# Performance work log

Measured on AMD Instinct MI355X. Metric: run time of the kernel, lower is better.

## Reference

```python
import jax, jax.numpy as jnp
import numpy as np


def _mlp(h, W1, b1, W2, b2):
    # Linear -> ReLU -> Linear
    h = jax.nn.relu(h @ W1 + b1)
    return h @ W2 + b2


def setup_inputs() -> dict:
    key = jax.random.key(0)
    ks = jax.random.split(key, 8)
    N, E, DN, DE, H, O = 50000, 800000, 128, 64, 256, 128
    DIN = DN + DE  # 192
    s1 = 1.0 / np.sqrt(DIN)
    s2 = 1.0 / np.sqrt(H)
    return {
        "x": jax.random.normal(ks[0], (N, DN), dtype=jnp.float32),
        "edge_index": jax.random.randint(ks[1], (2, E), 0, N, dtype=jnp.int32),
        "edge_attr": jax.random.normal(ks[2], (E, DE), dtype=jnp.float32),
        "W1_out": jax.random.normal(ks[3], (DIN, H), dtype=jnp.float32) * s1,
        "b1_out": jnp.zeros((H,), dtype=jnp.float32),
        "W2_out": jax.random.normal(ks[4], (H, O), dtype=jnp.float32) * s2,
        "b2_out": jnp.zeros((O,), dtype=jnp.float32),
        "W1_in": jax.random.normal(ks[5], (DIN, H), dtype=jnp.float32) * s1,
        "b1_in": jnp.zeros((H,), dtype=jnp.float32),
        "W2_in": jax.random.normal(ks[6], (H, O), dtype=jnp.float32) * s2,
        "b2_in": jnp.zeros((O,), dtype=jnp.float32),
    }


def reference(x, edge_index, edge_attr, W1_out, b1_out, W2_out, b2_out,
              W1_in, b1_in, W2_in, b2_in):
    N = x.shape[0]
    row, col = edge_index[0], edge_index[1]
    # Shared gather + concat: [E, d_node + d_edge]
    msg_in = jnp.concatenate([x[col], edge_attr], axis=1)

    # flow_out: edges with row < col. Compute MLP densely, zero masked edges,
    # then scatter-sum -> identical math to masked gather + scatter-sum.
    m_out = (row < col).astype(x.dtype)[:, None]
    flow_out = _mlp(msg_in, W1_out, b1_out, W2_out, b2_out) * m_out
    flow_out = jax.ops.segment_sum(flow_out, row, num_segments=N)

    # flow_in: edges with row > col
    m_in = (row > col).astype(x.dtype)[:, None]
    flow_in = _mlp(msg_in, W1_in, b1_in, W2_in, b2_in) * m_in
    flow_in = jax.ops.segment_sum(flow_in, row, num_segments=N)

    return jnp.concatenate((flow_in, flow_out), axis=1)  # [N, 2*O]
```

## Files before the change

kernel.cpp:

```cpp
#include <hip/hip_runtime.h>
#include <hip/hip_bf16.h>

typedef __attribute__((ext_vector_type(8))) short short8;
typedef __attribute__((ext_vector_type(4))) float f32x4;

#define DN   128
#define DE   64
#define DIN  192
#define HID  256
#define OUTD 128
#define TE   64
#define MSG_LD 200
#define H_LD   264
#define OUT_LD 132

static __device__ __forceinline__ unsigned short f2b(float f) {
    unsigned int u = __float_as_uint(f);
    u += 0x7fffu + ((u >> 16) & 1u);
    return (unsigned short)(u >> 16);
}

__global__ void pack_all_kernel(const float* __restrict__ W1o, const float* __restrict__ W1i,
                                const float* __restrict__ W2o, const float* __restrict__ W2i,
                                unsigned short* __restrict__ W1po, unsigned short* __restrict__ W1pi,
                                unsigned short* __restrict__ W2po, unsigned short* __restrict__ W2pi) {
    const int S1 = DIN * HID, S2 = HID * OUTD;
    int idx = blockIdx.x * blockDim.x + threadIdx.x;
    const float* W; unsigned short* Wp; int Ncols, j;
    if      (idx < S1)            { W = W1o; Wp = W1po; Ncols = HID;  j = idx; }
    else if (idx < 2*S1)          { W = W1i; Wp = W1pi; Ncols = HID;  j = idx - S1; }
    else if (idx < 2*S1 + S2)     { W = W2o; Wp = W2po; Ncols = OUTD; j = idx - 2*S1; }
    else if (idx < 2*S1 + 2*S2)   { W = W2i; Wp = W2pi; Ncols = OUTD; j = idx - 2*S1 - S2; }
    else return;
    int k = j / Ncols, n = j - k * Ncols;
    Wp[(((k >> 5) * Ncols + n) << 5) + (k & 31)] = f2b(W[j]);
}

__global__ __launch_bounds__(256)
void part_hist_kernel(const int* __restrict__ ei, int E, int N, int* __restrict__ hist) {
    int e = blockIdx.x * blockDim.x + threadIdx.x;
    if (e >= E) return;
    int r = ei[e], c = ei[E + e];
    if      (r < c) atomicAdd(&hist[r], 1);
    else if (r > c) atomicAdd(&hist[N + r], 1);
}

__global__ __launch_bounds__(1024)
void scan_kernel(const int* __restrict__ hist, int* __restrict__ cursor,
                 int* __restrict__ cnt, int N) {
    __shared__ int s_ws[16];
    __shared__ int s_run;
    const int tid = threadIdx.x, lane = tid & 63, wv = tid >> 6;
    const int b = blockIdx.x;
    const int* h = hist + (size_t)b * N;
    int* cu = cursor + (size_t)b * N;
    if (tid == 0) s_run = 0;
    __syncthreads();
    for (int base = 0; base < N; base += 1024) {
        int i = base + tid;
        int v = (i < N) ? h[i] : 0;
        int incl = v;
        #pragma unroll
        for (int d = 1; d < 64; d <<= 1) {
            int t = __shfl_up(incl, d, 64);
            if (lane >= d) incl += t;
        }
        if (lane == 63) s_ws[wv] = incl;
        __syncthreads();
        if (tid < 16) {
            int w = s_ws[tid];
            int wi = w;
            #pragma unroll
            for (int d = 1; d < 16; d <<= 1) {
                int t = __shfl_up(wi, d, 64);
                if (tid >= d) wi += t;
            }
            s_ws[tid] = wi - w;
        }
        __syncthreads();
        int excl = s_run + s_ws[wv] + incl - v;
        if (i < N) cu[i] = excl;
        __syncthreads();
        if (tid == 1023) s_run = excl + v;
        __syncthreads();
    }
    if (tid == 0) cnt[b] = s_run;
}

__global__ __launch_bounds__(256)
void reorder_kernel(const int* __restrict__ ei, int E, int N, int* __restrict__ cursor,
                    int* __restrict__ list_out, int* __restrict__ list_in) {
    int e = blockIdx.x * blockDim.x + threadIdx.x;
    if (e >= E) return;
    int r = ei[e], c = ei[E + e];
    if      (r < c) { int p = atomicAdd(&cursor[r], 1);            list_out[p] = e; }
    else if (r > c) { int p = atomicAdd(&cursor[(size_t)N + r], 1); list_in[p] = e; }
}

__global__ __launch_bounds__(256, 4)
void mlp_scatter_kernel(const float* __restrict__ x,
                        const int* __restrict__ ei,
                        const float* __restrict__ ea,
                        const unsigned short* __restrict__ W1p_out,
                        const unsigned short* __restrict__ W1p_in,
                        const float* __restrict__ b1_out,
                        const float* __restrict__ b1_in,
                        const unsigned short* __restrict__ W2p_out,
                        const unsigned short* __restrict__ W2p_in,
                        const float* __restrict__ b2_out,
                        const float* __restrict__ b2_in,
                        const int* __restrict__ list_out,
                        const int* __restrict__ list_in,
                        const int* __restrict__ cnt,
                        float* __restrict__ out,
                        int E, int nbpb) {
    __shared__ __align__(16) unsigned short s_buf[TE * H_LD];
    __shared__ int s_eid[TE], s_dest[TE], s_col[TE];

    const int branch = (blockIdx.x >= nbpb) ? 1 : 0;
    const int lb = blockIdx.x - branch * nbpb;
    const int count = cnt[branch];
    if (lb * TE >= count) return;
    const int* list            = branch ? list_in : list_out;
    const unsigned short* W1p  = branch ? W1p_in  : W1p_out;
    const float* b1            = branch ? b1_in   : b1_out;
    const unsigned short* W2p  = branch ? W2p_in  : W2p_out;
    const float* b2            = branch ? b2_in   : b2_out;
    const int colbase          = branch ? 0 : OUTD;

    const int tid = threadIdx.x;
    if (tid < TE) {
        int idx = lb * TE + tid;
        int e = (idx < count) ? list[idx] : -1;
        s_eid[tid]  = e;
        s_dest[tid] = (e >= 0) ? ei[e] : -1;
        s_col[tid]  = (e >= 0) ? ei[E + e] : 0;
    }
    __syncthreads();

    {
        const int le  = tid >> 2;
        const int sub = tid & 3;
        const int e   = s_eid[le];
        const long xbase = (long)s_col[le] * 32;
        const long ebase = (long)e * 16;
        #pragma unroll
        for (int j = 0; j < 12; ++j) {
            int q = sub + j * 4;
            float4 v = make_float4(0.f, 0.f, 0.f, 0.f);
            if (e >= 0) {
                if (j < 8) v = reinterpret_cast<const float4*>(x)[xbase + q];
                else       v = reinterpret_cast<const float4*>(ea)[ebase + (q - 32)];
            }
            unsigned int lo = (unsigned int)f2b(v.x) | ((unsigned int)f2b(v.y) << 16);
            unsigned int hi = (unsigned int)f2b(v.z) | ((unsigned int)f2b(v.w) << 16);
            *reinterpret_cast<uint2*>(&s_buf[le * MSG_LD + q * 4]) = make_uint2(lo, hi);
        }
    }
    __syncthreads();

    const int wave = tid >> 6;
    const int lane = tid & 63;
    const int ln   = lane & 15;
    const int quad = lane >> 4;

    f32x4 acc[4][4];
    {
        const int nbase = wave * 64;
        float bias[4];
        #pragma unroll
        for (int t = 0; t < 4; ++t) bias[t] = b1[nbase + t * 16 + ln];
        #pragma unroll
        for (int mt = 0; mt < 4; ++mt)
            #pragma unroll
            for (int t = 0; t < 4; ++t)
                acc[mt][t] = (f32x4){bias[t], bias[t], bias[t], bias[t]};
        #pragma unroll
        for (int kt = 0; kt < DIN / 32; ++kt) {
            short8 a[4], b[4];
            #pragma unroll
            for (int mt = 0; mt < 4; ++mt)
                a[mt] = *reinterpret_cast<const short8*>(
                    &s_buf[(mt * 16 + ln) * MSG_LD + kt * 32 + quad * 8]);
            #pragma unroll
            for (int t = 0; t < 4; ++t)
                b[t] = *reinterpret_cast<const short8*>(
                    &W1p[((kt * HID + nbase + t * 16 + ln) << 5) + quad * 8]);
            #pragma unroll
            for (int mt = 0; mt < 4; ++mt)
                #pragma unroll
                for (int t = 0; t < 4; ++t)
                    acc[mt][t] = __builtin_amdgcn_mfma_f32_16x16x32_bf16(a[mt], b[t], acc[mt][t], 0, 0, 0);
        }
    }
    __syncthreads();

    {
        const int nbase = wave * 64;
        #pragma unroll
        for (int mt = 0; mt < 4; ++mt)
            #pragma unroll
            for (int t = 0; t < 4; ++t) {
                int ncol = nbase + t * 16 + ln;
                #pragma unroll
                for (int r = 0; r < 4; ++r) {
                    int m = mt * 16 + quad * 4 + r;
                    float v = acc[mt][t][r];
                    s_buf[m * H_LD + ncol] = f2b(v > 0.f ? v : 0.f);
                }
            }
    }
    __syncthreads();

    f32x4 acc2[4][2];
    {
        const int nbase = wave * 32;
        float bias2[2];
        #pragma unroll
        for (int t = 0; t < 2; ++t) bias2[t] = b2[nbase + t * 16 + ln];
        #pragma unroll
        for (int mt = 0; mt < 4; ++mt)
            #pragma unroll
            for (int t = 0; t < 2; ++t)
                acc2[mt][t] = (f32x4){bias2[t], bias2[t], bias2[t], bias2[t]};
        #pragma unroll
        for (int kt = 0; kt < HID / 32; ++kt) {
            short8 a[4], b[2];
            #pragma unroll
            for (int mt = 0; mt < 4; ++mt)
                a[mt] = *reinterpret_cast<const short8*>(
                    &s_buf[(mt * 16 + ln) * H_LD + kt * 32 + quad * 8]);
            #pragma unroll
            for (int t = 0; t < 2; ++t)
                b[t] = *reinterpret_cast<const short8*>(
                    &W2p[((kt * OUTD + nbase + t * 16 + ln) << 5) + quad * 8]);
            #pragma unroll
            for (int mt = 0; mt < 4; ++mt)
                #pragma unroll
                for (int t = 0; t < 2; ++t)
                    acc2[mt][t] = __builtin_amdgcn_mfma_f32_16x16x32_bf16(a[mt], b[t], acc2[mt][t], 0, 0, 0);
        }
    }
    __syncthreads();

    float* s_outf = reinterpret_cast<float*>(s_buf);
    {
        const int nbase = wave * 32;
        #pragma unroll
        for (int mt = 0; mt < 4; ++mt)
            #pragma unroll
            for (int t = 0; t < 2; ++t)
                #pragma unroll
                for (int r = 0; r < 4; ++r)
                    s_outf[(mt * 16 + quad * 4 + r) * OUT_LD + nbase + t * 16 + ln] = acc2[mt][t][r];
    }
    __syncthreads();

    {
        const int c  = tid & 127;
        const int m0 = (tid >> 7) * 32;
        float run = 0.f;
        int cur = -1;
        #pragma unroll 8
        for (int m = m0; m < m0 + 32; ++m) {
            int d = s_dest[m];
            float v = s_outf[m * OUT_LD + c];
            if (d != cur) {
                if (cur >= 0) atomicAdd(&out[(size_t)cur * (2 * OUTD) + colbase + c], run);
                cur = d; run = 0.f;
            }
            if (d >= 0) run += v;
        }
        if (cur >= 0) atomicAdd(&out[(size_t)cur * (2 * OUTD) + colbase + c], run);
    }
}

extern "C" void kernel_launch(void* const* d_in, const int* in_sizes, int n_in,
                              void* d_out, int out_size, void* d_ws, size_t ws_size,
                              hipStream_t stream) {
    const float* x   = (const float*)d_in[0];
    const int*   ei  = (const int*)d_in[1];
    const float* ea  = (const float*)d_in[2];
    const float* W1o = (const float*)d_in[3];
    const float* b1o = (const float*)d_in[4];
    const float* W2o = (const float*)d_in[5];
    const float* b2o = (const float*)d_in[6];
    const float* W1i = (const float*)d_in[7];
    const float* b1i = (const float*)d_in[8];
    const float* W2i = (const float*)d_in[9];
    const float* b2i = (const float*)d_in[10];
    float* out = (float*)d_out;
    const int E = in_sizes[1] / 2;
    const int N = in_sizes[0] / DN;

    char* ws = (char*)d_ws;
    int* cnt      = (int*)ws;
    int* hist     = (int*)(ws + 64);
    int* cursor   = hist + 2 * (size_t)N;
    int* list_out = cursor + 2 * (size_t)N;
    int* list_in  = list_out + E;
    unsigned short* W1po = (unsigned short*)(list_in + E);
    unsigned short* W1pi = W1po + DIN * HID;
    unsigned short* W2po = W1pi + DIN * HID;
    unsigned short* W2pi = W2po + HID * OUTD;

    hipMemsetAsync(d_out, 0, (size_t)out_size * sizeof(float), stream);
    hipMemsetAsync(ws, 0, 64 + 2 * (size_t)N * sizeof(int), stream);

    const int packN = 2 * DIN * HID + 2 * HID * OUTD;
    pack_all_kernel<<<(packN + 255) / 256, 256, 0, stream>>>(
        W1o, W1i, W2o, W2i, W1po, W1pi, W2po, W2pi);

    part_hist_kernel<<<(E + 255) / 256, 256, 0, stream>>>(ei, E, N, hist);
    scan_kernel<<<2, 1024, 0, stream>>>(hist, cursor, cnt, N);
    reorder_kernel<<<(E + 255) / 256, 256, 0, stream>>>(ei, E, N, cursor, list_out, list_in);

    const int nbpb = (E + TE - 1) / TE;
    mlp_scatter_kernel<<<2 * nbpb, 256, 0, stream>>>(
        x, ei, ea, W1po, W1pi, b1o, b1i, W2po, W2pi, b2o, b2i,
        list_out, list_in, cnt, out, E, nbpb);
}
```

Measured before the change: 660.4 us.

## Pre-convert x to bf16, fuse prep kernels, parallelize scan, store interior segments

```diff
diff --git a/kernel.cpp b/kernel.cpp
--- a/kernel.cpp
+++ b/kernel.cpp
@@ -2,6 +2,7 @@
 #include <hip/hip_bf16.h>
 
 typedef __attribute__((ext_vector_type(8))) short short8;
+typedef __attribute__((ext_vector_type(8))) unsigned short ushort8;
 typedef __attribute__((ext_vector_type(4))) float f32x4;
 
 #define DN   128
@@ -20,85 +21,102 @@
     return (unsigned short)(u >> 16);
 }
 
-__global__ void pack_all_kernel(const float* __restrict__ W1o, const float* __restrict__ W1i,
-                                const float* __restrict__ W2o, const float* __restrict__ W2i,
-                                unsigned short* __restrict__ W1po, unsigned short* __restrict__ W1pi,
-                                unsigned short* __restrict__ W2po, unsigned short* __restrict__ W2pi) {
-    const int S1 = DIN * HID, S2 = HID * OUTD;
+__global__ __launch_bounds__(256)
+void prep_kernel(const float* __restrict__ W1o, const float* __restrict__ W1i,
+                 const float* __restrict__ W2o, const float* __restrict__ W2i,
+                 unsigned short* __restrict__ W1po, unsigned short* __restrict__ W1pi,
+                 unsigned short* __restrict__ W2po, unsigned short* __restrict__ W2pi,
+                 const int* __restrict__ ei, int E, int N, int* __restrict__ hist,
+                 const float* __restrict__ x, unsigned short* __restrict__ xb) {
+    const int S1 = DIN * HID, S2v = HID * OUTD;
+    const int PACKN = 2 * S1 + 2 * S2v;
     int idx = blockIdx.x * blockDim.x + threadIdx.x;
-    const float* W; unsigned short* Wp; int Ncols, j;
-    if      (idx < S1)            { W = W1o; Wp = W1po; Ncols = HID;  j = idx; }
-    else if (idx < 2*S1)          { W = W1i; Wp = W1pi; Ncols = HID;  j = idx - S1; }
-    else if (idx < 2*S1 + S2)     { W = W2o; Wp = W2po; Ncols = OUTD; j = idx - 2*S1; }
-    else if (idx < 2*S1 + 2*S2)   { W = W2i; Wp = W2pi; Ncols = OUTD; j = idx - 2*S1 - S2; }
-    else return;
-    int k = j / Ncols, n = j - k * Ncols;
-    Wp[(((k >> 5) * Ncols + n) << 5) + (k & 31)] = f2b(W[j]);
+    if (idx < PACKN) {
+        const float* W; unsigned short* Wp; int Nc, j;
+        if      (idx < S1)          { W = W1o; Wp = W1po; Nc = HID;  j = idx; }
+        else if (idx < 2*S1)        { W = W1i; Wp = W1pi; Nc = HID;  j = idx - S1; }
+        else if (idx < 2*S1 + S2v)  { W = W2o; Wp = W2po; Nc = OUTD; j = idx - 2*S1; }
+        else                        { W = W2i; Wp = W2pi; Nc = OUTD; j = idx - 2*S1 - S2v; }
+        int k = j / Nc, n = j - k * Nc;
+        Wp[(((k >> 5) * Nc + n) << 5) + (k & 31)] = f2b(W[j]);
+    } else if (idx < PACKN + E) {
+        int e = idx - PACKN;
+        int r = ei[e], c = ei[E + e];
+        if      (r < c) atomicAdd(&hist[r], 1);
+        else if (r > c) atomicAdd(&hist[N + r], 1);
+    } else {
+        int i = idx - PACKN - E;
+        if (i < N * DN / 8) {
+            float4 a = reinterpret_cast<const float4*>(x)[i * 2];
+            float4 b = reinterpret_cast<const float4*>(x)[i * 2 + 1];
+            ushort8 v = { f2b(a.x), f2b(a.y), f2b(a.z), f2b(a.w),
+                          f2b(b.x), f2b(b.y), f2b(b.z), f2b(b.w) };
+            reinterpret_cast<ushort8*>(xb)[i] = v;
+        }
+    }
+}
+
+__global__ __launch_bounds__(1024)
+void scan1_kernel(const int* __restrict__ hist, int* __restrict__ cursor,
+                  int* __restrict__ chunkSum, int N, int nch) {
+    __shared__ int s_ws[16];
+    const int br = blockIdx.x / nch, ch = blockIdx.x - br * nch;
+    const int tid = threadIdx.x, lane = tid & 63, wv = tid >> 6;
+    const int i = ch * 1024 + tid;
+    int v = (i < N) ? hist[(size_t)br * N + i] : 0;
+    int incl = v;
+    #pragma unroll
+    for (int d = 1; d < 64; d <<= 1) {
+        int t = __shfl_up(incl, d, 64);
+        if (lane >= d) incl += t;
+    }
+    if (lane == 63) s_ws[wv] = incl;
+    __syncthreads();
+    if (tid < 16) {
+        int w = s_ws[tid];
+        int wi = w;
+        #pragma unroll
+        for (int d = 1; d < 16; d <<= 1) {
+            int t = __shfl_up(wi, d, 64);
+            if (tid >= d) wi += t;
+        }
+        s_ws[tid] = wi - w;
+    }
+    __syncthreads();
+    int excl = s_ws[wv] + incl - v;
+    if (i < N) cursor[(size_t)br * N + i] = excl;
+    if (tid == 1023) chunkSum[br * nch + ch] = excl + v;
+}
+
+__global__ __launch_bounds__(128)
+void scan2_kernel(int* __restrict__ chunkSum, int* __restrict__ cnt, int nch) {
+    const int br = threadIdx.x >> 6, lane = threadIdx.x & 63;
+    int v = (lane < nch) ? chunkSum[br * nch + lane] : 0;
+    int incl = v;
+    #pragma unroll
+    for (int d = 1; d < 64; d <<= 1) {
+        int t = __shfl_up(incl, d, 64);
+        if (lane >= d) incl += t;
+    }
+    if (lane < nch) chunkSum[br * nch + lane] = incl - v;
+    if (lane == nch - 1) cnt[br] = incl;
 }
 
 __global__ __launch_bounds__(256)
-void part_hist_kernel(const int* __restrict__ ei, int E, int N, int* __restrict__ hist) {
-    int e = blockIdx.x * blockDim.x + threadIdx.x;
-    if (e >= E) return;
-    int r = ei[e], c = ei[E + e];
-    if      (r < c) atomicAdd(&hist[r], 1);
-    else if (r > c) atomicAdd(&hist[N + r], 1);
-}
-
-__global__ __launch_bounds__(1024)
-void scan_kernel(const int* __restrict__ hist, int* __restrict__ cursor,
-                 int* __restrict__ cnt, int N) {
-    __shared__ int s_ws[16];
-    __shared__ int s_run;
-    const int tid = threadIdx.x, lane = tid & 63, wv = tid >> 6;
-    const int b = blockIdx.x;
-    const int* h = hist + (size_t)b * N;
-    int* cu = cursor + (size_t)b * N;
-    if (tid == 0) s_run = 0;
-    __syncthreads();
-    for (int base = 0; base < N; base += 1024) {
-        int i = base + tid;
-        int v = (i < N) ? h[i] : 0;
-        int incl = v;
-        #pragma unroll
-        for (int d = 1; d < 64; d <<= 1) {
-            int t = __shfl_up(incl, d, 64);
-            if (lane >= d) incl += t;
-        }
-        if (lane == 63) s_ws[wv] = incl;
-        __syncthreads();
-        if (tid < 16) {
-            int w = s_ws[tid];
-            int wi = w;
-            #pragma unroll
-            for (int d = 1; d < 16; d <<= 1) {
-                int t = __shfl_up(wi, d, 64);
-                if (tid >= d) wi += t;
-            }
-            s_ws[tid] = wi - w;
-        }
-        __syncthreads();
-        int excl = s_run + s_ws[wv] + incl - v;
-        if (i < N) cu[i] = excl;
-        __syncthreads();
-        if (tid == 1023) s_run = excl + v;
-        __syncthreads();
-    }
-    if (tid == 0) cnt[b] = s_run;
-}
-
-__global__ __launch_bounds__(256)
-void reorder_kernel(const int* __restrict__ ei, int E, int N, int* __restrict__ cursor,
+void reorder_kernel(const int* __restrict__ ei, int E, int N, int nch,
+                    int* __restrict__ cursor, const int* __restrict__ chunkSum,
                     int* __restrict__ list_out, int* __restrict__ list_in) {
     int e = blockIdx.x * blockDim.x + threadIdx.x;
     if (e >= E) return;
     int r = ei[e], c = ei[E + e];
-    if      (r < c) { int p = atomicAdd(&cursor[r], 1);            list_out[p] = e; }
-    else if (r > c) { int p = atomicAdd(&cursor[(size_t)N + r], 1); list_in[p] = e; }
+    if (r == c) return;
+    int br = (r < c) ? 0 : 1;
+    int p = chunkSum[br * nch + (r >> 10)] + atomicAdd(&cursor[(size_t)br * N + r], 1);
+    (br ? list_in : list_out)[p] = e;
 }
 
 __global__ __launch_bounds__(256, 4)
-void mlp_scatter_kernel(const float* __restrict__ x,
+void mlp_scatter_kernel(const unsigned short* __restrict__ xb,
                         const int* __restrict__ ei,
                         const float* __restrict__ ea,
                         const unsigned short* __restrict__ W1p_out,
@@ -142,19 +160,22 @@
         const int le  = tid >> 2;
         const int sub = tid & 3;
         const int e   = s_eid[le];
-        const long xbase = (long)s_col[le] * 32;
-        const long ebase = (long)e * 16;
-        #pragma unroll
-        for (int j = 0; j < 12; ++j) {
-            int q = sub + j * 4;
+        const ushort8* xrow = reinterpret_cast<const ushort8*>(xb) + (size_t)s_col[le] * (DN / 8);
+        #pragma unroll
+        for (int j = 0; j < 4; ++j) {
+            int seg = sub + j * 4;
+            ushort8 v = {0, 0, 0, 0, 0, 0, 0, 0};
+            if (e >= 0) v = xrow[seg];
+            *reinterpret_cast<ushort8*>(&s_buf[le * MSG_LD + seg * 8]) = v;
+        }
+        const float4* erow = reinterpret_cast<const float4*>(ea) + (size_t)e * (DE / 4);
+        #pragma unroll
+        for (int j = 0; j < 4; ++j) {
             float4 v = make_float4(0.f, 0.f, 0.f, 0.f);
-            if (e >= 0) {
-                if (j < 8) v = reinterpret_cast<const float4*>(x)[xbase + q];
-                else       v = reinterpret_cast<const float4*>(ea)[ebase + (q - 32)];
-            }
+            if (e >= 0) v = erow[sub * 4 + j];
             unsigned int lo = (unsigned int)f2b(v.x) | ((unsigned int)f2b(v.y) << 16);
             unsigned int hi = (unsigned int)f2b(v.z) | ((unsigned int)f2b(v.w) << 16);
-            *reinterpret_cast<uint2*>(&s_buf[le * MSG_LD + q * 4]) = make_uint2(lo, hi);
+            *reinterpret_cast<uint2*>(&s_buf[le * MSG_LD + DN + sub * 16 + j * 4]) = make_uint2(lo, hi);
         }
     }
     __syncthreads();
@@ -260,18 +281,21 @@
         const int c  = tid & 127;
         const int m0 = (tid >> 7) * 32;
         float run = 0.f;
-        int cur = -1;
-        #pragma unroll 8
+        int cur = -1, rs = m0;
         for (int m = m0; m < m0 + 32; ++m) {
             int d = s_dest[m];
             float v = s_outf[m * OUT_LD + c];
             if (d != cur) {
-                if (cur >= 0) atomicAdd(&out[(size_t)cur * (2 * OUTD) + colbase + c], run);
-                cur = d; run = 0.f;
+                if (cur >= 0) {
+                    float* p = &out[(size_t)cur * (2 * OUTD) + colbase + c];
+                    if (rs > m0) *p = run; else atomicAdd(p, run);
+                }
+                cur = d; run = 0.f; rs = m;
             }
             if (d >= 0) run += v;
         }
-        if (cur >= 0) atomicAdd(&out[(size_t)cur * (2 * OUTD) + colbase + c], run);
+        if (cur >= 0)
+            atomicAdd(&out[(size_t)cur * (2 * OUTD) + colbase + c], run);
     }
 }
 
@@ -292,10 +316,11 @@
     float* out = (float*)d_out;
     const int E = in_sizes[1] / 2;
     const int N = in_sizes[0] / DN;
-
-    char* ws = (char*)d_ws;
-    int* cnt      = (int*)ws;
-    int* hist     = (int*)(ws + 64);
+    const int nch = (N + 1023) >> 10;
+
+    int* cnt      = (int*)d_ws;
+    int* chunkSum = cnt + 16;
+    int* hist     = chunkSum + 128;
     int* cursor   = hist + 2 * (size_t)N;
     int* list_out = cursor + 2 * (size_t)N;
     int* list_in  = list_out + E;
@@ -303,20 +328,23 @@
     unsigned short* W1pi = W1po + DIN * HID;
     unsigned short* W2po = W1pi + DIN * HID;
     unsigned short* W2pi = W2po + HID * OUTD;
+    unsigned short* xb   = W2pi + HID * OUTD;
 
     hipMemsetAsync(d_out, 0, (size_t)out_size * sizeof(float), stream);
-    hipMemsetAsync(ws, 0, 64 + 2 * (size_t)N * sizeof(int), stream);
-
-    const int packN = 2 * DIN * HID + 2 * HID * OUTD;
-    pack_all_kernel<<<(packN + 255) / 256, 256, 0, stream>>>(
-        W1o, W1i, W2o, W2i, W1po, W1pi, W2po, W2pi);
-
-    part_hist_kernel<<<(E + 255) / 256, 256, 0, stream>>>(ei, E, N, hist);
-    scan_kernel<<<2, 1024, 0, stream>>>(hist, cursor, cnt, N);
-    reorder_kernel<<<(E + 255) / 256, 256, 0, stream>>>(ei, E, N, cursor, list_out, list_in);
+    hipMemsetAsync(d_ws, 0, (576 + 8 * (size_t)N), stream);
+
+    const int PACKN = 2 * DIN * HID + 2 * HID * OUTD;
+    const int prepN = PACKN + E + N * DN / 8;
+    prep_kernel<<<(prepN + 255) / 256, 256, 0, stream>>>(
+        W1o, W1i, W2o, W2i, W1po, W1pi, W2po, W2pi, ei, E, N, hist, x, xb);
+
+    scan1_kernel<<<2 * nch, 1024, 0, stream>>>(hist, cursor, chunkSum, N, nch);
+    scan2_kernel<<<1, 128, 0, stream>>>(chunkSum, cnt, nch);
+    reorder_kernel<<<(E + 255) / 256, 256, 0, stream>>>(
+        ei, E, N, nch, cursor, chunkSum, list_out, list_in);
 
     const int nbpb = (E + TE - 1) / TE;
     mlp_scatter_kernel<<<2 * nbpb, 256, 0, stream>>>(
-        x, ei, ea, W1po, W1pi, b1o, b1i, W2po, W2pi, b2o, b2i,
+        xb, ei, ea, W1po, W1pi, b1o, b1i, W2po, W2pi, b2o, b2i,
         list_out, list_in, cnt, out, E, nbpb);
 }
```

Result: faster. 603.5 us (-8.6%).
